# Optimization experiments

Hardware: AMD Instinct MI355X
Metric: run time of the kernel (lower is better)

Reference implementation:

```python
import jax, jax.numpy as jnp
import numpy as np

N_NODES = 50000
IN_DIM = 5000
OUT_DIM = 128
NNZ_X = 1000000
NNZ_ADJ = 1600000


def setup_inputs() -> dict:
    key = jax.random.key(0)
    k1, k2, k3, k4, k5, k6, k7 = jax.random.split(key, 7)
    x_rows = jax.random.randint(k1, (NNZ_X,), 0, N_NODES, dtype=jnp.int32)
    x_cols = jax.random.randint(k2, (NNZ_X,), 0, IN_DIM, dtype=jnp.int32)
    x_vals = jax.random.normal(k3, (NNZ_X,), dtype=jnp.float32)
    adj_rows = jax.random.randint(k4, (NNZ_ADJ,), 0, N_NODES, dtype=jnp.int32)
    adj_cols = jax.random.randint(k5, (NNZ_ADJ,), 0, N_NODES, dtype=jnp.int32)
    adj_vals = jax.random.uniform(k6, (NNZ_ADJ,), dtype=jnp.float32)
    # Glorot-uniform init as in weight_variable_glorot
    init_range = np.sqrt(6.0 / (IN_DIM + OUT_DIM))
    W = jax.random.uniform(k7, (IN_DIM, OUT_DIM), dtype=jnp.float32,
                           minval=-init_range, maxval=init_range)
    return {"x_rows": x_rows, "x_cols": x_cols, "x_vals": x_vals,
            "adj_rows": adj_rows, "adj_cols": adj_cols, "adj_vals": adj_vals,
            "W": W}


def reference(x_rows, x_cols, x_vals, adj_rows, adj_cols, adj_vals, W):
    # dropout = 0 -> sparse dropout is identity (keep_prob = 1).
    # Step 1: xw = sparse_x @ W  -> [N, D] via gather rows of W + segment sum over node ids
    xw = jax.ops.segment_sum(x_vals[:, None] * W[x_cols], x_rows,
                             num_segments=N_NODES)  # [N, D]
    # Step 2: out = sparse_adj @ xw  -> gather neighbor features, weight, scatter-add
    agg = jax.ops.segment_sum(adj_vals[:, None] * xw[adj_cols], adj_rows,
                              num_segments=N_NODES)  # [N, D]
    return jax.nn.relu(agg)
```

## Files before the change

kernel.cpp:

```cpp
#include <hip/hip_runtime.h>

#define ODIM 128
#define BROWS 128
#define NBMAX 512
#define TILE 4096
#define CMASK 0x1FFFFu

typedef unsigned u32;


__global__ __launch_bounds__(256) void hist_buckets(
    const int* __restrict__ xr, int nx, const int* __restrict__ ar, int na,
    int* __restrict__ ghX, int* __restrict__ ghA) {
  __shared__ int lh[2 * NBMAX];
  for (int i = threadIdx.x; i < 2 * NBMAX; i += 256) lh[i] = 0;
  __syncthreads();
  int total = nx + na;
  for (int i = blockIdx.x * 256 + threadIdx.x; i < total; i += gridDim.x * 256) {
    if (i < nx) atomicAdd(&lh[xr[i] >> 7], 1);
    else        atomicAdd(&lh[NBMAX + (ar[i - nx] >> 7)], 1);
  }
  __syncthreads();
  for (int b = threadIdx.x; b < NBMAX; b += 256) {
    if (lh[b])         atomicAdd(&ghX[b], lh[b]);
    if (lh[NBMAX + b]) atomicAdd(&ghA[b], lh[NBMAX + b]);
  }
}


__global__ __launch_bounds__(NBMAX) void scan_buckets(
    int* __restrict__ ghX, int* __restrict__ baseX, int* __restrict__ curX,
    int* __restrict__ ghA, int* __restrict__ baseA, int* __restrict__ curA,
    int nb) {
  int* gh   = blockIdx.x ? ghA   : ghX;
  int* base = blockIdx.x ? baseA : baseX;
  int* cur  = blockIdx.x ? curA  : curX;
  __shared__ int s[NBMAX];
  int tid = threadIdx.x;
  int v = (tid < nb) ? gh[tid] : 0;
  s[tid] = v;
  __syncthreads();
  for (int off = 1; off < NBMAX; off <<= 1) {
    int t = (tid >= off) ? s[tid - off] : 0;
    __syncthreads();
    s[tid] += t;
    __syncthreads();
  }
  int excl = s[tid] - v;
  if (tid < nb) { base[tid] = excl; cur[tid] = excl; }
  if (tid == NBMAX - 1) base[nb] = s[tid];
}


__device__ inline unsigned f2bf(float x) {
  unsigned u = __float_as_uint(x);
  return (u + 0x7fffu + ((u >> 16) & 1u)) >> 16;
}

__global__ __launch_bounds__(256) void conv_w(
    const float2* __restrict__ W2, u32* __restrict__ Wbf, int nwords) {
  int i = blockIdx.x * 256 + threadIdx.x;
  if (i >= nwords) return;
  float2 w = W2[i];
  Wbf[i] = f2bf(w.x) | (f2bf(w.y) << 16);
}


__global__ __launch_bounds__(256) void partition_both(
    const int* __restrict__ xr, const int* __restrict__ xc,
    const float* __restrict__ xv, int nx, int ntX,
    int* __restrict__ curX, uint2* __restrict__ outX,
    const int* __restrict__ ar, const int* __restrict__ ac,
    const float* __restrict__ av, int na,
    int* __restrict__ curA, uint2* __restrict__ outA) {
  __shared__ uint2 pay[TILE];
  __shared__ unsigned short bkt[TILE];
  __shared__ unsigned short perm[TILE];
  __shared__ int hist[NBMAX];
  __shared__ int scn[NBMAX];
  __shared__ int cur[NBMAX];
  __shared__ int gbase[NBMAX];
  __shared__ int part[256];

  const int* rows; const int* cols; const float* vals;
  int nnz; int* gcur; uint2* outbuf; int tile;
  if ((int)blockIdx.x < ntX) {
    rows = xr; cols = xc; vals = xv; nnz = nx; gcur = curX; outbuf = outX;
    tile = blockIdx.x;
  } else {
    rows = ar; cols = ac; vals = av; nnz = na; gcur = curA; outbuf = outA;
    tile = blockIdx.x - ntX;
  }

  int tid = threadIdx.x;
  int tbase = tile * TILE;
  int cnt = nnz - tbase; if (cnt > TILE) cnt = TILE;

  for (int b = tid; b < NBMAX; b += 256) hist[b] = 0;
  __syncthreads();

  for (int j = tid; j < cnt; j += 256) {
    int r = rows[tbase + j];
    int c = cols[tbase + j];
    float v = vals[tbase + j];
    unsigned b = (unsigned)r >> 7;
    bkt[j] = (unsigned short)b;
    pay[j] = make_uint2(((unsigned)(r & 127) << 17) | (unsigned)c, __float_as_uint(v));
    atomicAdd(&hist[b], 1);
  }
  __syncthreads();

  int h0 = hist[2 * tid], h1 = hist[2 * tid + 1];
  int psum = h0 + h1;
  part[tid] = psum;
  __syncthreads();
  for (int off = 1; off < 256; off <<= 1) {
    int t = (tid >= off) ? part[tid - off] : 0;
    __syncthreads();
    part[tid] += t;
    __syncthreads();
  }
  int excl = part[tid] - psum;
  scn[2 * tid] = excl;     scn[2 * tid + 1] = excl + h0;
  cur[2 * tid] = excl;     cur[2 * tid + 1] = excl + h0;
  __syncthreads();

  for (int j = tid; j < cnt; j += 256) {
    int pos = atomicAdd(&cur[bkt[j]], 1);
    perm[pos] = (unsigned short)j;
  }
  for (int b = tid; b < NBMAX; b += 256) {
    int c = hist[b];
    if (c) gbase[b] = atomicAdd(&gcur[b], c);
  }
  __syncthreads();

  for (int p = tid; p < cnt; p += 256) {
    int j = perm[p];
    int b = bkt[j];
    outbuf[gbase[b] + (p - scn[b])] = pay[j];
  }
}


__global__ __launch_bounds__(256) void bucket_sort_both(
    int nbX,
    const int* __restrict__ baseX, const uint2* __restrict__ binX,
    uint2* __restrict__ boutX, int* __restrict__ rpX,
    const int* __restrict__ baseA, const uint2* __restrict__ binA,
    uint2* __restrict__ boutA, int* __restrict__ rpA, int N) {
  __shared__ int hist[BROWS], scn[BROWS], cur[BROWS];
  const int* base; const uint2* bufin; uint2* bufout; int* rowptr; int b;
  if ((int)blockIdx.x < nbX) {
    base = baseX; bufin = binX; bufout = boutX; rowptr = rpX; b = blockIdx.x;
  } else {
    base = baseA; bufin = binA; bufout = boutA; rowptr = rpA; b = blockIdx.x - nbX;
  }
  int tid = threadIdx.x;
  int e0 = base[b], ecnt = base[b + 1] - e0;

  if (tid < BROWS) hist[tid] = 0;
  __syncthreads();
  for (int j = tid; j < ecnt; j += 256)
    atomicAdd(&hist[bufin[e0 + j].x >> 17], 1);
  __syncthreads();

  int v = (tid < BROWS) ? hist[tid] : 0;
  if (tid < BROWS) scn[tid] = v;
  __syncthreads();
  for (int off = 1; off < BROWS; off <<= 1) {
    int t = (tid < BROWS && tid >= off) ? scn[tid - off] : 0;
    __syncthreads();
    if (tid < BROWS) scn[tid] += t;
    __syncthreads();
  }
  if (tid < BROWS) {
    int excl = scn[tid] - v;
    cur[tid] = excl;
    int node = b * BROWS + tid;
    if (node <= N) rowptr[node] = e0 + excl;
  }
  __syncthreads();

  for (int j = tid; j < ecnt; j += 256) {
    uint2 e = bufin[e0 + j];
    int pos = atomicAdd(&cur[e.x >> 17], 1);
    bufout[e0 + pos] = e;
  }
}


__global__ __launch_bounds__(256) void pull_x(
    const int* __restrict__ rowptr, const uint2* __restrict__ cv,
    const u32* __restrict__ Wbf, unsigned* __restrict__ xw, int nrows) {
  int lane = threadIdx.x & 63;
  int r = blockIdx.x * 4 + (threadIdx.x >> 6);
  if (r >= nrows) return;
  int e = rowptr[r], end = rowptr[r + 1];
  float acc0[8], acc1[8];
#pragma unroll
  for (int u = 0; u < 8; ++u) { acc0[u] = 0.f; acc1[u] = 0.f; }
  for (; e + 7 < end; e += 8) {
    uint2 ed[8]; unsigned xg[8];
#pragma unroll
    for (int u = 0; u < 8; ++u) ed[u] = cv[e + u];
#pragma unroll
    for (int u = 0; u < 8; ++u)
      xg[u] = Wbf[(size_t)(ed[u].x & CMASK) * 64 + lane];
#pragma unroll
    for (int u = 0; u < 8; ++u) {
      float v = __uint_as_float(ed[u].y);
      acc0[u] += v * __uint_as_float(xg[u] << 16);
      acc1[u] += v * __uint_as_float(xg[u] & 0xffff0000u);
    }
  }
  for (; e + 1 < end; e += 2) {
    uint2 ea = cv[e], eb = cv[e + 1];
    unsigned ua = Wbf[(size_t)(ea.x & CMASK) * 64 + lane];
    unsigned ub = Wbf[(size_t)(eb.x & CMASK) * 64 + lane];
    float va = __uint_as_float(ea.y), vb = __uint_as_float(eb.y);
    acc0[0] += va * __uint_as_float(ua << 16);
    acc1[0] += va * __uint_as_float(ua & 0xffff0000u);
    acc0[1] += vb * __uint_as_float(ub << 16);
    acc1[1] += vb * __uint_as_float(ub & 0xffff0000u);
  }
  if (e < end) {
    uint2 ea = cv[e];
    unsigned ua = Wbf[(size_t)(ea.x & CMASK) * 64 + lane];
    float va = __uint_as_float(ea.y);
    acc0[2] += va * __uint_as_float(ua << 16);
    acc1[2] += va * __uint_as_float(ua & 0xffff0000u);
  }
  float o0 = ((acc0[0] + acc0[1]) + (acc0[2] + acc0[3])) +
             ((acc0[4] + acc0[5]) + (acc0[6] + acc0[7]));
  float o1 = ((acc1[0] + acc1[1]) + (acc1[2] + acc1[3])) +
             ((acc1[4] + acc1[5]) + (acc1[6] + acc1[7]));
  xw[(size_t)r * 64 + lane] = f2bf(o0) | (f2bf(o1) << 16);
}

__global__ __launch_bounds__(256) void pull_a(
    const int* __restrict__ rowptr, const uint2* __restrict__ cv,
    const unsigned* __restrict__ xw, float2* __restrict__ out, int nrows) {
  int lane = threadIdx.x & 63;
  int r = blockIdx.x * 4 + (threadIdx.x >> 6);
  if (r >= nrows) return;
  int e = rowptr[r], end = rowptr[r + 1];
  float acc0[8], acc1[8];
#pragma unroll
  for (int u = 0; u < 8; ++u) { acc0[u] = 0.f; acc1[u] = 0.f; }
  for (; e + 7 < end; e += 8) {
    uint2 ed[8]; unsigned xg[8];
#pragma unroll
    for (int u = 0; u < 8; ++u) ed[u] = cv[e + u];
#pragma unroll
    for (int u = 0; u < 8; ++u)
      xg[u] = xw[(size_t)(ed[u].x & CMASK) * 64 + lane];
#pragma unroll
    for (int u = 0; u < 8; ++u) {
      float v = __uint_as_float(ed[u].y);
      acc0[u] += v * __uint_as_float(xg[u] << 16);
      acc1[u] += v * __uint_as_float(xg[u] & 0xffff0000u);
    }
  }
  for (; e + 1 < end; e += 2) {
    uint2 ea = cv[e], eb = cv[e + 1];
    unsigned ua = xw[(size_t)(ea.x & CMASK) * 64 + lane];
    unsigned ub = xw[(size_t)(eb.x & CMASK) * 64 + lane];
    float va = __uint_as_float(ea.y), vb = __uint_as_float(eb.y);
    acc0[0] += va * __uint_as_float(ua << 16);
    acc1[0] += va * __uint_as_float(ua & 0xffff0000u);
    acc0[1] += vb * __uint_as_float(ub << 16);
    acc1[1] += vb * __uint_as_float(ub & 0xffff0000u);
  }
  if (e < end) {
    uint2 ea = cv[e];
    unsigned ua = xw[(size_t)(ea.x & CMASK) * 64 + lane];
    float va = __uint_as_float(ea.y);
    acc0[2] += va * __uint_as_float(ua << 16);
    acc1[2] += va * __uint_as_float(ua & 0xffff0000u);
  }
  float o0 = ((acc0[0] + acc0[1]) + (acc0[2] + acc0[3])) +
             ((acc0[4] + acc0[5]) + (acc0[6] + acc0[7]));
  float o1 = ((acc1[0] + acc1[1]) + (acc1[2] + acc1[3])) +
             ((acc1[4] + acc1[5]) + (acc1[6] + acc1[7]));
  out[(size_t)r * 64 + lane] = make_float2(fmaxf(o0, 0.f), fmaxf(o1, 0.f));
}


__global__ __launch_bounds__(256) void spmm_scatter(
    const int* __restrict__ rows, const int* __restrict__ cols,
    const float* __restrict__ vals, const float* __restrict__ B,
    float* __restrict__ out, int nnz) {
  int e = blockIdx.x * 2 + (threadIdx.x >> 7);
  int d = threadIdx.x & (ODIM - 1);
  if (e >= nnz) return;
  atomicAdd(&out[(size_t)rows[e] * ODIM + d],
            vals[e] * B[(size_t)cols[e] * ODIM + d]);
}

__global__ __launch_bounds__(256) void relu_inplace(float* __restrict__ p, long n4) {
  long i = (long)blockIdx.x * blockDim.x + threadIdx.x;
  long stride = (long)gridDim.x * blockDim.x;
  float4* p4 = (float4*)p;
  for (long j = i; j < n4; j += stride) {
    float4 v = p4[j];
    v.x = fmaxf(v.x, 0.f); v.y = fmaxf(v.y, 0.f);
    v.z = fmaxf(v.z, 0.f); v.w = fmaxf(v.w, 0.f);
    p4[j] = v;
  }
}

extern "C" void kernel_launch(void* const* d_in, const int* in_sizes, int n_in,
                              void* d_out, int out_size, void* d_ws, size_t ws_size,
                              hipStream_t stream) {
  const int*   x_rows   = (const int*)d_in[0];
  const int*   x_cols   = (const int*)d_in[1];
  const float* x_vals   = (const float*)d_in[2];
  const int*   adj_rows = (const int*)d_in[3];
  const int*   adj_cols = (const int*)d_in[4];
  const float* adj_vals = (const float*)d_in[5];
  const float* W        = (const float*)d_in[6];

  const int nnz_x   = in_sizes[0];
  const int nnz_adj = in_sizes[3];
  const int wlen    = in_sizes[6];
  const int N       = out_size / ODIM;
  const int NB      = (N + BROWS - 1) / BROWS;
  const int ntX     = (nnz_x + TILE - 1) / TILE;
  const int ntA     = (nnz_adj + TILE - 1) / TILE;
  const int wwords  = wlen / 2;

  float* out = (float*)d_out;

  char* p = (char*)d_ws;
  int* ghX   = (int*)p;  p += NBMAX * sizeof(int);
  int* ghA   = (int*)p;  p += NBMAX * sizeof(int);
  int* baseX = (int*)p;  p += (NBMAX + 1) * sizeof(int);
  int* baseA = (int*)p;  p += (NBMAX + 1) * sizeof(int);
  int* curX  = (int*)p;  p += NBMAX * sizeof(int);
  int* curA  = (int*)p;  p += NBMAX * sizeof(int);
  int* rpX   = (int*)p;  p += (size_t)(N + 1) * sizeof(int);
  int* rpA   = (int*)p;  p += (size_t)(N + 1) * sizeof(int);
  p = (char*)(((uintptr_t)p + 255) & ~(uintptr_t)255);
  u32* Wbf   = (u32*)p;  p += (size_t)wwords * sizeof(u32);
  p = (char*)(((uintptr_t)p + 255) & ~(uintptr_t)255);
  char* bufs = p;

  const size_t xw_bytes = (size_t)N * 64 * sizeof(u32);

  {
    char* q = bufs;
    uint2* bufPX = (uint2*)q; q += (size_t)nnz_x * sizeof(uint2);
    uint2* bufPA = (uint2*)q; q += (size_t)nnz_adj * sizeof(uint2);
    uint2* bufSX = (uint2*)q; q += (size_t)nnz_x * sizeof(uint2);
    uint2* bufSA = (uint2*)q; q += (size_t)nnz_adj * sizeof(uint2);
    size_t need = (size_t)(q - (char*)d_ws);
    bool xw_fits = xw_bytes <= ((size_t)nnz_x + nnz_adj) * sizeof(uint2);
    if (ws_size >= need && NB <= NBMAX && xw_fits) {
      u32* xw = (u32*)bufPX;
      (void)hipMemsetAsync(ghX, 0, 2 * NBMAX * sizeof(int), stream);
      hist_buckets<<<1024, 256, 0, stream>>>(x_rows, nnz_x, adj_rows, nnz_adj, ghX, ghA);
      conv_w<<<(wwords + 255) / 256, 256, 0, stream>>>((const float2*)W, Wbf, wwords);
      scan_buckets<<<2, NBMAX, 0, stream>>>(ghX, baseX, curX, ghA, baseA, curA, NB);
      partition_both<<<ntX + ntA, 256, 0, stream>>>(
          x_rows, x_cols, x_vals, nnz_x, ntX, curX, bufPX,
          adj_rows, adj_cols, adj_vals, nnz_adj, curA, bufPA);
      bucket_sort_both<<<2 * NB, 256, 0, stream>>>(
          NB, baseX, bufPX, bufSX, rpX, baseA, bufPA, bufSA, rpA, N);
      pull_x<<<(N + 3) / 4, 256, 0, stream>>>(rpX, bufSX, Wbf, xw, N);
      pull_a<<<(N + 3) / 4, 256, 0, stream>>>(rpA, bufSA, xw, (float2*)out, N);
      return;
    }
  }

  {
    size_t bufP_elems = (size_t)(nnz_x > nnz_adj ? nnz_x : nnz_adj);
    if (bufP_elems * sizeof(uint2) < xw_bytes)
      bufP_elems = (xw_bytes + sizeof(uint2) - 1) / sizeof(uint2);
    char* q = bufs;
    uint2* bufP  = (uint2*)q; q += bufP_elems * sizeof(uint2);
    uint2* bufSX = (uint2*)q; q += (size_t)nnz_x * sizeof(uint2);
    uint2* bufSA = (uint2*)q; q += (size_t)nnz_adj * sizeof(uint2);
    size_t need = (size_t)(q - (char*)d_ws);
    if (ws_size >= need && NB <= NBMAX) {
      u32* xw = (u32*)bufP;
      (void)hipMemsetAsync(ghX, 0, 2 * NBMAX * sizeof(int), stream);
      hist_buckets<<<1024, 256, 0, stream>>>(x_rows, nnz_x, adj_rows, nnz_adj, ghX, ghA);
      conv_w<<<(wwords + 255) / 256, 256, 0, stream>>>((const float2*)W, Wbf, wwords);
      scan_buckets<<<2, NBMAX, 0, stream>>>(ghX, baseX, curX, ghA, baseA, curA, NB);
      partition_both<<<ntX, 256, 0, stream>>>(
          x_rows, x_cols, x_vals, nnz_x, ntX, curX, bufP,
          adj_rows, adj_cols, adj_vals, nnz_adj, curA, bufP);
      bucket_sort_both<<<NB, 256, 0, stream>>>(
          NB, baseX, bufP, bufSX, rpX, baseA, bufP, bufSA, rpA, N);
      partition_both<<<ntA, 256, 0, stream>>>(
          x_rows, x_cols, x_vals, nnz_x, 0, curX, bufP,
          adj_rows, adj_cols, adj_vals, nnz_adj, curA, bufP);
      bucket_sort_both<<<NB, 256, 0, stream>>>(
          0, baseX, bufP, bufSX, rpX, baseA, bufP, bufSA, rpA, N);
      pull_x<<<(N + 3) / 4, 256, 0, stream>>>(rpX, bufSX, Wbf, xw, N);
      pull_a<<<(N + 3) / 4, 256, 0, stream>>>(rpA, bufSA, xw, (float2*)out, N);
      return;
    }
  }

  {
    float* xwf = (float*)d_ws;
    const size_t out_bytes = (size_t)out_size * sizeof(float);
    (void)hipMemsetAsync(xwf, 0, out_bytes, stream);
    (void)hipMemsetAsync(out, 0, out_bytes, stream);
    spmm_scatter<<<(nnz_x + 1) / 2, 256, 0, stream>>>(x_rows, x_cols, x_vals, W, xwf, nnz_x);
    spmm_scatter<<<(nnz_adj + 1) / 2, 256, 0, stream>>>(adj_rows, adj_cols, adj_vals, xwf, out, nnz_adj);
    relu_inplace<<<2048, 256, 0, stream>>>(out, (long)out_size / 4);
  }
}
```

Measured before the change: 173.8 us.

## Fuse preprocessing kernels into one persistent kernel with grid barriers

Merges the histogram, W bf16 conversion, bucket scan, partition and per-bucket sort stages into a single persistent kernel of 512 blocks separated by software grid barriers. The aim is to remove the launch gaps and tail effects between several small kernels. Tile size shrinks to 2560 so the shared-memory footprint fits 40KB and allows two blocks per CU. It drops the lower-memory fallback path, and the spin barriers assume all 512 blocks are co-resident, so the kernel could deadlock if they are not.

```diff
diff --git a/kernel.cpp b/kernel.cpp
--- a/kernel.cpp
+++ b/kernel.cpp
@@ -3,189 +3,199 @@
 #define ODIM 128
 #define BROWS 128
 #define NBMAX 512
-#define TILE 4096
+#define TILE 2560
 #define CMASK 0x1FFFFu
+#define PREP_GRID 512
+#define PREP_THREADS 256
 
 typedef unsigned u32;
-
-
-__global__ __launch_bounds__(256) void hist_buckets(
-    const int* __restrict__ xr, int nx, const int* __restrict__ ar, int na,
-    int* __restrict__ ghX, int* __restrict__ ghA) {
-  __shared__ int lh[2 * NBMAX];
-  for (int i = threadIdx.x; i < 2 * NBMAX; i += 256) lh[i] = 0;
-  __syncthreads();
-  int total = nx + na;
-  for (int i = blockIdx.x * 256 + threadIdx.x; i < total; i += gridDim.x * 256) {
-    if (i < nx) atomicAdd(&lh[xr[i] >> 7], 1);
-    else        atomicAdd(&lh[NBMAX + (ar[i - nx] >> 7)], 1);
-  }
-  __syncthreads();
-  for (int b = threadIdx.x; b < NBMAX; b += 256) {
-    if (lh[b])         atomicAdd(&ghX[b], lh[b]);
-    if (lh[NBMAX + b]) atomicAdd(&ghA[b], lh[NBMAX + b]);
-  }
-}
-
-
-__global__ __launch_bounds__(NBMAX) void scan_buckets(
-    int* __restrict__ ghX, int* __restrict__ baseX, int* __restrict__ curX,
-    int* __restrict__ ghA, int* __restrict__ baseA, int* __restrict__ curA,
-    int nb) {
-  int* gh   = blockIdx.x ? ghA   : ghX;
-  int* base = blockIdx.x ? baseA : baseX;
-  int* cur  = blockIdx.x ? curA  : curX;
-  __shared__ int s[NBMAX];
-  int tid = threadIdx.x;
-  int v = (tid < nb) ? gh[tid] : 0;
-  s[tid] = v;
-  __syncthreads();
-  for (int off = 1; off < NBMAX; off <<= 1) {
-    int t = (tid >= off) ? s[tid - off] : 0;
-    __syncthreads();
-    s[tid] += t;
-    __syncthreads();
-  }
-  int excl = s[tid] - v;
-  if (tid < nb) { base[tid] = excl; cur[tid] = excl; }
-  if (tid == NBMAX - 1) base[nb] = s[tid];
-}
-
 
 __device__ inline unsigned f2bf(float x) {
   unsigned u = __float_as_uint(x);
   return (u + 0x7fffu + ((u >> 16) & 1u)) >> 16;
 }
 
-__global__ __launch_bounds__(256) void conv_w(
-    const float2* __restrict__ W2, u32* __restrict__ Wbf, int nwords) {
-  int i = blockIdx.x * 256 + threadIdx.x;
-  if (i >= nwords) return;
-  float2 w = W2[i];
-  Wbf[i] = f2bf(w.x) | (f2bf(w.y) << 16);
-}
-
-
-__global__ __launch_bounds__(256) void partition_both(
+__device__ inline void grid_bar(unsigned* cnt, unsigned nblk) {
+  __syncthreads();
+  if (threadIdx.x == 0) {
+    __threadfence();
+    unsigned arrived =
+        __hip_atomic_fetch_add(cnt, 1u, __ATOMIC_ACQ_REL, __HIP_MEMORY_SCOPE_AGENT) + 1u;
+    if (arrived < nblk) {
+      while (__hip_atomic_load(cnt, __ATOMIC_ACQUIRE, __HIP_MEMORY_SCOPE_AGENT) < nblk)
+        __builtin_amdgcn_s_sleep(2);
+    }
+  }
+  __syncthreads();
+}
+
+__global__ __launch_bounds__(PREP_THREADS, 2) void prep_all(
     const int* __restrict__ xr, const int* __restrict__ xc,
-    const float* __restrict__ xv, int nx, int ntX,
-    int* __restrict__ curX, uint2* __restrict__ outX,
+    const float* __restrict__ xv, int nx,
     const int* __restrict__ ar, const int* __restrict__ ac,
     const float* __restrict__ av, int na,
-    int* __restrict__ curA, uint2* __restrict__ outA) {
-  __shared__ uint2 pay[TILE];
-  __shared__ unsigned short bkt[TILE];
-  __shared__ unsigned short perm[TILE];
-  __shared__ int hist[NBMAX];
-  __shared__ int scn[NBMAX];
-  __shared__ int cur[NBMAX];
-  __shared__ int gbase[NBMAX];
-  __shared__ int part[256];
-
-  const int* rows; const int* cols; const float* vals;
-  int nnz; int* gcur; uint2* outbuf; int tile;
-  if ((int)blockIdx.x < ntX) {
-    rows = xr; cols = xc; vals = xv; nnz = nx; gcur = curX; outbuf = outX;
-    tile = blockIdx.x;
-  } else {
-    rows = ar; cols = ac; vals = av; nnz = na; gcur = curA; outbuf = outA;
-    tile = blockIdx.x - ntX;
-  }
-
-  int tid = threadIdx.x;
-  int tbase = tile * TILE;
-  int cnt = nnz - tbase; if (cnt > TILE) cnt = TILE;
-
-  for (int b = tid; b < NBMAX; b += 256) hist[b] = 0;
-  __syncthreads();
-
-  for (int j = tid; j < cnt; j += 256) {
-    int r = rows[tbase + j];
-    int c = cols[tbase + j];
-    float v = vals[tbase + j];
-    unsigned b = (unsigned)r >> 7;
-    bkt[j] = (unsigned short)b;
-    pay[j] = make_uint2(((unsigned)(r & 127) << 17) | (unsigned)c, __float_as_uint(v));
-    atomicAdd(&hist[b], 1);
-  }
-  __syncthreads();
-
-  int h0 = hist[2 * tid], h1 = hist[2 * tid + 1];
-  int psum = h0 + h1;
-  part[tid] = psum;
-  __syncthreads();
-  for (int off = 1; off < 256; off <<= 1) {
-    int t = (tid >= off) ? part[tid - off] : 0;
+    const float2* __restrict__ W2, u32* __restrict__ Wbf, int wwords,
+    int* __restrict__ ghX, int* __restrict__ ghA,
+    int* __restrict__ baseX, int* __restrict__ baseA,
+    int* __restrict__ curX, int* __restrict__ curA,
+    uint2* __restrict__ bufPX, uint2* __restrict__ bufPA,
+    uint2* __restrict__ bufSX, uint2* __restrict__ bufSA,
+    int* __restrict__ rpX, int* __restrict__ rpA,
+    int N, int nb, int ntX, int ntA, unsigned* __restrict__ bars) {
+  __shared__ __align__(16) char smem[40960];
+  const int tid = threadIdx.x;
+  const int bid = blockIdx.x;
+  const int gsize = PREP_GRID * PREP_THREADS;
+  const int gtid = bid * PREP_THREADS + tid;
+
+  for (int i = gtid; i < 2 * NBMAX; i += gsize) {
+    if (i < NBMAX) ghX[i] = 0;
+    else           ghA[i - NBMAX] = 0;
+  }
+  for (int i = gtid; i < wwords; i += gsize) {
+    float2 w = W2[i];
+    Wbf[i] = f2bf(w.x) | (f2bf(w.y) << 16);
+  }
+  grid_bar(&bars[0], PREP_GRID);
+
+  {
+    int* lh = (int*)smem;
+    for (int i = tid; i < 2 * NBMAX; i += PREP_THREADS) lh[i] = 0;
     __syncthreads();
-    part[tid] += t;
+    int total = nx + na;
+    for (int i = gtid; i < total; i += gsize) {
+      if (i < nx) atomicAdd(&lh[xr[i] >> 7], 1);
+      else        atomicAdd(&lh[NBMAX + (ar[i - nx] >> 7)], 1);
+    }
     __syncthreads();
-  }
-  int excl = part[tid] - psum;
-  scn[2 * tid] = excl;     scn[2 * tid + 1] = excl + h0;
-  cur[2 * tid] = excl;     cur[2 * tid + 1] = excl + h0;
-  __syncthreads();
-
-  for (int j = tid; j < cnt; j += 256) {
-    int pos = atomicAdd(&cur[bkt[j]], 1);
-    perm[pos] = (unsigned short)j;
-  }
-  for (int b = tid; b < NBMAX; b += 256) {
-    int c = hist[b];
-    if (c) gbase[b] = atomicAdd(&gcur[b], c);
-  }
-  __syncthreads();
-
-  for (int p = tid; p < cnt; p += 256) {
-    int j = perm[p];
-    int b = bkt[j];
-    outbuf[gbase[b] + (p - scn[b])] = pay[j];
-  }
-}
-
-
-__global__ __launch_bounds__(256) void bucket_sort_both(
-    int nbX,
-    const int* __restrict__ baseX, const uint2* __restrict__ binX,
-    uint2* __restrict__ boutX, int* __restrict__ rpX,
-    const int* __restrict__ baseA, const uint2* __restrict__ binA,
-    uint2* __restrict__ boutA, int* __restrict__ rpA, int N) {
-  __shared__ int hist[BROWS], scn[BROWS], cur[BROWS];
-  const int* base; const uint2* bufin; uint2* bufout; int* rowptr; int b;
-  if ((int)blockIdx.x < nbX) {
-    base = baseX; bufin = binX; bufout = boutX; rowptr = rpX; b = blockIdx.x;
-  } else {
-    base = baseA; bufin = binA; bufout = boutA; rowptr = rpA; b = blockIdx.x - nbX;
-  }
-  int tid = threadIdx.x;
-  int e0 = base[b], ecnt = base[b + 1] - e0;
-
-  if (tid < BROWS) hist[tid] = 0;
-  __syncthreads();
-  for (int j = tid; j < ecnt; j += 256)
-    atomicAdd(&hist[bufin[e0 + j].x >> 17], 1);
-  __syncthreads();
-
-  int v = (tid < BROWS) ? hist[tid] : 0;
-  if (tid < BROWS) scn[tid] = v;
-  __syncthreads();
-  for (int off = 1; off < BROWS; off <<= 1) {
-    int t = (tid < BROWS && tid >= off) ? scn[tid - off] : 0;
+    for (int b = tid; b < NBMAX; b += PREP_THREADS) {
+      if (lh[b])         atomicAdd(&ghX[b], lh[b]);
+      if (lh[NBMAX + b]) atomicAdd(&ghA[b], lh[NBMAX + b]);
+    }
+  }
+  grid_bar(&bars[1], PREP_GRID);
+
+  if (bid < 2) {
+    int* gh   = bid ? ghA   : ghX;
+    int* base = bid ? baseA : baseX;
+    int* cur  = bid ? curA  : curX;
+    int* s = (int*)smem;
+    int h0 = gh[2 * tid], h1 = gh[2 * tid + 1];
+    int psum = h0 + h1;
+    s[tid] = psum;
     __syncthreads();
-    if (tid < BROWS) scn[tid] += t;
-    __syncthreads();
-  }
-  if (tid < BROWS) {
-    int excl = scn[tid] - v;
-    cur[tid] = excl;
-    int node = b * BROWS + tid;
-    if (node <= N) rowptr[node] = e0 + excl;
-  }
-  __syncthreads();
-
-  for (int j = tid; j < ecnt; j += 256) {
-    uint2 e = bufin[e0 + j];
-    int pos = atomicAdd(&cur[e.x >> 17], 1);
-    bufout[e0 + pos] = e;
+    for (int off = 1; off < 256; off <<= 1) {
+      int t = (tid >= off) ? s[tid - off] : 0;
+      __syncthreads();
+      s[tid] += t;
+      __syncthreads();
+    }
+    int excl = s[tid] - psum;
+    base[2 * tid] = excl;     base[2 * tid + 1] = excl + h0;
+    cur[2 * tid]  = excl;     cur[2 * tid + 1]  = excl + h0;
+    if (tid == 255) base[NBMAX] = s[255];
+  }
+  grid_bar(&bars[2], PREP_GRID);
+
+  {
+    uint2* pay           = (uint2*)smem;
+    unsigned short* bkt  = (unsigned short*)(smem + 20480);
+    unsigned short* perm = (unsigned short*)(smem + 25600);
+    int* hist            = (int*)(smem + 30720);
+    int* scn             = (int*)(smem + 32768);
+    int* lcur            = (int*)(smem + 34816);
+    int* gbase           = (int*)(smem + 36864);
+    int* part            = (int*)(smem + 38912);
+    const int ntot = ntX + ntA;
+    for (int t = bid; t < ntot; t += PREP_GRID) {
+      const int* rows; const int* cols; const float* vals;
+      int nnz; int* gcur; uint2* outbuf; int tile;
+      if (t < ntX) { rows = xr; cols = xc; vals = xv; nnz = nx; gcur = curX; outbuf = bufPX; tile = t; }
+      else         { rows = ar; cols = ac; vals = av; nnz = na; gcur = curA; outbuf = bufPA; tile = t - ntX; }
+      int tbase = tile * TILE;
+      int cnt = nnz - tbase; if (cnt > TILE) cnt = TILE;
+      __syncthreads();
+      for (int b = tid; b < NBMAX; b += PREP_THREADS) hist[b] = 0;
+      __syncthreads();
+      for (int j = tid; j < cnt; j += PREP_THREADS) {
+        int r = rows[tbase + j];
+        int c = cols[tbase + j];
+        float v = vals[tbase + j];
+        unsigned bb = (unsigned)r >> 7;
+        bkt[j] = (unsigned short)bb;
+        pay[j] = make_uint2(((unsigned)(r & 127) << 17) | (unsigned)c, __float_as_uint(v));
+        atomicAdd(&hist[bb], 1);
+      }
+      __syncthreads();
+      int h0 = hist[2 * tid], h1 = hist[2 * tid + 1];
+      int psum = h0 + h1;
+      part[tid] = psum;
+      __syncthreads();
+      for (int off = 1; off < 256; off <<= 1) {
+        int tv = (tid >= off) ? part[tid - off] : 0;
+        __syncthreads();
+        part[tid] += tv;
+        __syncthreads();
+      }
+      int excl = part[tid] - psum;
+      scn[2 * tid] = excl;    scn[2 * tid + 1] = excl + h0;
+      lcur[2 * tid] = excl;   lcur[2 * tid + 1] = excl + h0;
+      __syncthreads();
+      for (int j = tid; j < cnt; j += PREP_THREADS) {
+        int pos = atomicAdd(&lcur[bkt[j]], 1);
+        perm[pos] = (unsigned short)j;
+      }
+      for (int b = tid; b < NBMAX; b += PREP_THREADS) {
+        int c2 = hist[b];
+        if (c2) gbase[b] = atomicAdd(&gcur[b], c2);
+      }
+      __syncthreads();
+      for (int pp = tid; pp < cnt; pp += PREP_THREADS) {
+        int j = perm[pp];
+        int bb = bkt[j];
+        outbuf[gbase[bb] + (pp - scn[bb])] = pay[j];
+      }
+    }
+  }
+  grid_bar(&bars[3], PREP_GRID);
+
+  {
+    int* hist = (int*)smem;
+    int* scn  = (int*)(smem + 512);
+    int* lcur = (int*)(smem + 1024);
+    for (int u2 = bid; u2 < 2 * nb; u2 += PREP_GRID) {
+      const int* bbase; const uint2* bin; uint2* bout; int* rowptr; int b;
+      if (u2 < nb) { bbase = baseX; bin = bufPX; bout = bufSX; rowptr = rpX; b = u2; }
+      else         { bbase = baseA; bin = bufPA; bout = bufSA; rowptr = rpA; b = u2 - nb; }
+      int e0 = bbase[b], ecnt = bbase[b + 1] - e0;
+      __syncthreads();
+      if (tid < BROWS) hist[tid] = 0;
+      __syncthreads();
+      for (int j = tid; j < ecnt; j += PREP_THREADS)
+        atomicAdd(&hist[bin[e0 + j].x >> 17], 1);
+      __syncthreads();
+      int v = (tid < BROWS) ? hist[tid] : 0;
+      if (tid < BROWS) scn[tid] = v;
+      __syncthreads();
+      for (int off = 1; off < BROWS; off <<= 1) {
+        int tt = (tid < BROWS && tid >= off) ? scn[tid - off] : 0;
+        __syncthreads();
+        if (tid < BROWS) scn[tid] += tt;
+        __syncthreads();
+      }
+      if (tid < BROWS) {
+        int excl = scn[tid] - v;
+        lcur[tid] = excl;
+        int node = b * BROWS + tid;
+        if (node <= N) rowptr[node] = e0 + excl;
+      }
+      __syncthreads();
+      for (int j = tid; j < ecnt; j += PREP_THREADS) {
+        uint2 e = bin[e0 + j];
+        int pos = atomicAdd(&lcur[e.x >> 17], 1);
+        bout[e0 + pos] = e;
+      }
+    }
   }
 }
 
@@ -333,6 +343,7 @@
   float* out = (float*)d_out;
 
   char* p = (char*)d_ws;
+  unsigned* bars = (unsigned*)p; p += 256;
   int* ghX   = (int*)p;  p += NBMAX * sizeof(int);
   int* ghA   = (int*)p;  p += NBMAX * sizeof(int);
   int* baseX = (int*)p;  p += (NBMAX + 1) * sizeof(int);
@@ -344,64 +355,28 @@
   p = (char*)(((uintptr_t)p + 255) & ~(uintptr_t)255);
   u32* Wbf   = (u32*)p;  p += (size_t)wwords * sizeof(u32);
   p = (char*)(((uintptr_t)p + 255) & ~(uintptr_t)255);
-  char* bufs = p;
+  uint2* bufPX = (uint2*)p; p += (size_t)nnz_x * sizeof(uint2);
+  uint2* bufPA = (uint2*)p; p += (size_t)nnz_adj * sizeof(uint2);
+  uint2* bufSX = (uint2*)p; p += (size_t)nnz_x * sizeof(uint2);
+  uint2* bufSA = (uint2*)p; p += (size_t)nnz_adj * sizeof(uint2);
+  size_t need = (size_t)(p - (char*)d_ws);
 
   const size_t xw_bytes = (size_t)N * 64 * sizeof(u32);
-
-  {
-    char* q = bufs;
-    uint2* bufPX = (uint2*)q; q += (size_t)nnz_x * sizeof(uint2);
-    uint2* bufPA = (uint2*)q; q += (size_t)nnz_adj * sizeof(uint2);
-    uint2* bufSX = (uint2*)q; q += (size_t)nnz_x * sizeof(uint2);
-    uint2* bufSA = (uint2*)q; q += (size_t)nnz_adj * sizeof(uint2);
-    size_t need = (size_t)(q - (char*)d_ws);
-    bool xw_fits = xw_bytes <= ((size_t)nnz_x + nnz_adj) * sizeof(uint2);
-    if (ws_size >= need && NB <= NBMAX && xw_fits) {
-      u32* xw = (u32*)bufPX;
-      (void)hipMemsetAsync(ghX, 0, 2 * NBMAX * sizeof(int), stream);
-      hist_buckets<<<1024, 256, 0, stream>>>(x_rows, nnz_x, adj_rows, nnz_adj, ghX, ghA);
-      conv_w<<<(wwords + 255) / 256, 256, 0, stream>>>((const float2*)W, Wbf, wwords);
-      scan_buckets<<<2, NBMAX, 0, stream>>>(ghX, baseX, curX, ghA, baseA, curA, NB);
-      partition_both<<<ntX + ntA, 256, 0, stream>>>(
-          x_rows, x_cols, x_vals, nnz_x, ntX, curX, bufPX,
-          adj_rows, adj_cols, adj_vals, nnz_adj, curA, bufPA);
-      bucket_sort_both<<<2 * NB, 256, 0, stream>>>(
-          NB, baseX, bufPX, bufSX, rpX, baseA, bufPA, bufSA, rpA, N);
-      pull_x<<<(N + 3) / 4, 256, 0, stream>>>(rpX, bufSX, Wbf, xw, N);
-      pull_a<<<(N + 3) / 4, 256, 0, stream>>>(rpA, bufSA, xw, (float2*)out, N);
-      return;
-    }
-  }
-
-  {
-    size_t bufP_elems = (size_t)(nnz_x > nnz_adj ? nnz_x : nnz_adj);
-    if (bufP_elems * sizeof(uint2) < xw_bytes)
-      bufP_elems = (xw_bytes + sizeof(uint2) - 1) / sizeof(uint2);
-    char* q = bufs;
-    uint2* bufP  = (uint2*)q; q += bufP_elems * sizeof(uint2);
-    uint2* bufSX = (uint2*)q; q += (size_t)nnz_x * sizeof(uint2);
-    uint2* bufSA = (uint2*)q; q += (size_t)nnz_adj * sizeof(uint2);
-    size_t need = (size_t)(q - (char*)d_ws);
-    if (ws_size >= need && NB <= NBMAX) {
-      u32* xw = (u32*)bufP;
-      (void)hipMemsetAsync(ghX, 0, 2 * NBMAX * sizeof(int), stream);
-      hist_buckets<<<1024, 256, 0, stream>>>(x_rows, nnz_x, adj_rows, nnz_adj, ghX, ghA);
-      conv_w<<<(wwords + 255) / 256, 256, 0, stream>>>((const float2*)W, Wbf, wwords);
-      scan_buckets<<<2, NBMAX, 0, stream>>>(ghX, baseX, curX, ghA, baseA, curA, NB);
-      partition_both<<<ntX, 256, 0, stream>>>(
-          x_rows, x_cols, x_vals, nnz_x, ntX, curX, bufP,
-          adj_rows, adj_cols, adj_vals, nnz_adj, curA, bufP);
-      bucket_sort_both<<<NB, 256, 0, stream>>>(
-          NB, baseX, bufP, bufSX, rpX, baseA, bufP, bufSA, rpA, N);
-      partition_both<<<ntA, 256, 0, stream>>>(
-          x_rows, x_cols, x_vals, nnz_x, 0, curX, bufP,
-          adj_rows, adj_cols, adj_vals, nnz_adj, curA, bufP);
-      bucket_sort_both<<<NB, 256, 0, stream>>>(
-          0, baseX, bufP, bufSX, rpX, baseA, bufP, bufSA, rpA, N);
-      pull_x<<<(N + 3) / 4, 256, 0, stream>>>(rpX, bufSX, Wbf, xw, N);
-      pull_a<<<(N + 3) / 4, 256, 0, stream>>>(rpA, bufSA, xw, (float2*)out, N);
-      return;
-    }
+  bool xw_fits = xw_bytes <= ((size_t)nnz_x + nnz_adj) * sizeof(uint2);
+
+  if (ws_size >= need && NB <= NBMAX && xw_fits) {
+    u32* xw = (u32*)bufPX;
+    (void)hipMemsetAsync(bars, 0, 4 * sizeof(unsigned), stream);
+    prep_all<<<PREP_GRID, PREP_THREADS, 0, stream>>>(
+        x_rows, x_cols, x_vals, nnz_x,
+        adj_rows, adj_cols, adj_vals, nnz_adj,
+        (const float2*)W, Wbf, wwords,
+        ghX, ghA, baseX, baseA, curX, curA,
+        bufPX, bufPA, bufSX, bufSA, rpX, rpA,
+        N, NB, ntX, ntA, bars);
+    pull_x<<<(N + 3) / 4, 256, 0, stream>>>(rpX, bufSX, Wbf, xw, N);
+    pull_a<<<(N + 3) / 4, 256, 0, stream>>>(rpA, bufSA, xw, (float2*)out, N);
+    return;
   }
 
   {
```

Measured after the change: 321.0 us. 84.7% more time.
